# Optimization experiments

Measured on AMD Instinct MI355X. Metric: run time of the kernel, lower is better.

## Reference

```python
import jax, jax.numpy as jnp
import numpy as np

N_NODES, N_EDGES, N_ROOTS = 32768, 131072, 1024
VOCAB, EMB_D, FEAT = 50000, 256, 128
SEQ, HEADS, OUT_CH = 16, 16, 125
KERNELS = (5, 6, 7, 8)


def _add_self_loops(edge_index, n):
    loop = jnp.arange(n, dtype=edge_index.dtype)
    src = jnp.concatenate([edge_index[0], loop])
    dst = jnp.concatenate([edge_index[1], loop])
    return src, dst


def _gat_conv(x, W, a_src, a_dst, b, src, dst, n):
    # PyG GATConv (heads=1): h=xW, e_ij = LeakyReLU(a_s.h_j + a_d.h_i), softmax over incoming edges of i
    h = x @ W                                   # [N, F]
    al_s = h @ a_src                            # [N]
    al_d = h @ a_dst                            # [N]
    e = jax.nn.leaky_relu(al_s[src] + al_d[dst], 0.2)   # [E+N]
    m = jax.ops.segment_max(e, dst, num_segments=n)
    ex = jnp.exp(e - m[dst])
    den = jax.ops.segment_sum(ex, dst, num_segments=n)
    coef = ex / den[dst]
    out = jax.ops.segment_sum(coef[:, None] * h[src], dst, num_segments=n)
    return out + b


def _gcn_conv(x, W, b, src, dst, n):
    h = x @ W
    ones = jnp.ones_like(src, dtype=x.dtype)
    deg = jax.ops.segment_sum(ones, dst, num_segments=n)
    dinv = jax.lax.rsqrt(jnp.maximum(deg, 1.0))
    norm = dinv[src] * dinv[dst]                # [E+N]
    out = jax.ops.segment_sum(norm[:, None] * h[src], dst, num_segments=n)
    return out + b


def _transformer_block(x, Wq, bq, Wk, bk, Wv, bv, Wo, bo, g, be):
    # multi-head self-attention + output proj + residual + layernorm (attn_dropout=0)
    n, s, d = x.shape
    dh = d // HEADS
    q = (x @ Wq + bq).reshape(n, s, HEADS, dh)
    k = (x @ Wk + bk).reshape(n, s, HEADS, dh)
    v = (x @ Wv + bv).reshape(n, s, HEADS, dh)
    att = jnp.einsum('nqhd,nkhd->nhqk', q, k) / np.sqrt(dh).astype(np.float32)
    att = jax.nn.softmax(att, axis=-1)
    o = jnp.einsum('nhqk,nkhd->nqhd', att, v).reshape(n, s, d)
    o = o @ Wo + bo
    y = x + o
    mu = jnp.mean(y, axis=-1, keepdims=True)
    var = jnp.var(y, axis=-1, keepdims=True)
    return (y - mu) * jax.lax.rsqrt(var + 1e-5) * g + be


def _conv_branch(t, ws, bs):
    # t: [N, D, S]; Conv1d VALID + ReLU + max-pool over full output length
    feats = []
    for w, b in zip(ws, bs):
        a = jax.lax.conv_general_dilated(t, w, (1,), 'VALID',
                                         dimension_numbers=('NCH', 'OIH', 'NCH'))
        a = jax.nn.relu(a + b[:, None])
        feats.append(jnp.max(a, axis=-1))       # [N, OUT_CH]
    return jnp.concatenate(feats, axis=1)        # [N, 4*OUT_CH]


def _forward(x2, emb, Wq, bq, Wk, bk, Wv, bv, Wo, bo, ln_g, ln_b,
             gat1_W, gat1_as, gat1_ad, gat1_b, gcn1_W, gcn1_b,
             gat2_W, gat2_as, gat2_ad, gat2_b, gcn2_W, gcn2_b,
             conv_w0, conv_b0, conv_w1, conv_b1, conv_w2, conv_b2, conv_w3, conv_b3,
             fc1_W, fc1_b, fc2_W, fc2_b,
             text2, edge_index, root_index, rootpost_index):
    n = x2.shape[0]
    src, dst = _add_self_loops(edge_index, n)

    stance_graph = _gat_conv(x2, gat1_W, gat1_as, gat1_ad, gat1_b, src, dst, n)
    stance_shared = _gcn_conv(x2, gcn1_W, gcn1_b, src, dst, n)

    t = emb[text2]                                            # [N, S, D]
    t = _transformer_block(t, Wq, bq, Wk, bk, Wv, bv, Wo, bo, ln_g, ln_b)
    t_avg = jnp.mean(t, axis=1)                               # [N, D]

    cat = jnp.concatenate([stance_graph, stance_shared, t_avg], axis=1)  # [N, 2F+D]
    stance_graph2 = _gat_conv(cat, gat2_W, gat2_as, gat2_ad, gat2_b, src, dst, n)
    _ = _gcn_conv(stance_shared, gcn2_W, gcn2_b, src, dst, n)  # computed but unused in forward (faithful)

    tc = jnp.transpose(t, (0, 2, 1))                          # [N, D, S]
    text_feat = _conv_branch(tc, (conv_w0, conv_w1, conv_w2, conv_w3),
                             (conv_b0, conv_b1, conv_b2, conv_b3))  # [N, 500]

    final = jnp.concatenate([stance_graph2[root_index],
                             text_feat[root_index],
                             text_feat[rootpost_index]], axis=1)     # [B, F+1000]
    h = jax.nn.relu(final @ fc1_W + fc1_b)
    return h @ fc2_W + fc2_b                                  # [B, 3]


def setup_inputs() -> dict:
    key = jax.random.key(0)
    ks = iter(jax.random.split(key, 48))
    s = 0.05
    inp = {}
    inp['x2'] = jax.random.normal(next(ks), (N_NODES, FEAT), jnp.float32)
    inp['emb'] = jax.random.normal(next(ks), (VOCAB, EMB_D), jnp.float32) * s
    for nm in ['Wq', 'Wk', 'Wv', 'Wo']:
        inp[nm] = jax.random.normal(next(ks), (EMB_D, EMB_D), jnp.float32) * s
    for nm in ['bq', 'bk', 'bv', 'bo']:
        inp[nm] = jnp.zeros((EMB_D,), jnp.float32)
    inp['ln_g'] = jnp.ones((EMB_D,), jnp.float32)
    inp['ln_b'] = jnp.zeros((EMB_D,), jnp.float32)
    inp['gat1_W'] = jax.random.normal(next(ks), (FEAT, FEAT), jnp.float32) * s
    inp['gat1_as'] = jax.random.normal(next(ks), (FEAT,), jnp.float32) * s
    inp['gat1_ad'] = jax.random.normal(next(ks), (FEAT,), jnp.float32) * s
    inp['gat1_b'] = jnp.zeros((FEAT,), jnp.float32)
    inp['gcn1_W'] = jax.random.normal(next(ks), (FEAT, FEAT), jnp.float32) * s
    inp['gcn1_b'] = jnp.zeros((FEAT,), jnp.float32)
    inp['gat2_W'] = jax.random.normal(next(ks), (2 * FEAT + EMB_D, FEAT), jnp.float32) * s
    inp['gat2_as'] = jax.random.normal(next(ks), (FEAT,), jnp.float32) * s
    inp['gat2_ad'] = jax.random.normal(next(ks), (FEAT,), jnp.float32) * s
    inp['gat2_b'] = jnp.zeros((FEAT,), jnp.float32)
    inp['gcn2_W'] = jax.random.normal(next(ks), (FEAT, FEAT), jnp.float32) * s
    inp['gcn2_b'] = jnp.zeros((FEAT,), jnp.float32)
    for i, K in enumerate(KERNELS):
        inp[f'conv_w{i}'] = jax.random.normal(next(ks), (OUT_CH, EMB_D, K), jnp.float32) * s
        inp[f'conv_b{i}'] = jnp.zeros((OUT_CH,), jnp.float32)
    inp['fc1_W'] = jax.random.normal(next(ks), (FEAT + 8 * OUT_CH, 300), jnp.float32) * s
    inp['fc1_b'] = jnp.zeros((300,), jnp.float32)
    inp['fc2_W'] = jax.random.normal(next(ks), (300, 3), jnp.float32) * s
    inp['fc2_b'] = jnp.zeros((3,), jnp.float32)
    inp['text2'] = jax.random.randint(next(ks), (N_NODES, SEQ), 0, VOCAB, jnp.int32)
    inp['edge_index'] = jax.random.randint(next(ks), (2, N_EDGES), 0, N_NODES, jnp.int32)
    inp['root_index'] = jax.random.randint(next(ks), (N_ROOTS,), 0, N_NODES, jnp.int32)
    inp['rootpost_index'] = jax.random.randint(next(ks), (N_ROOTS,), 0, N_NODES, jnp.int32)
    return inp


def reference(x2, emb, Wq, bq, Wk, bk, Wv, bv, Wo, bo, ln_g, ln_b,
              gat1_W, gat1_as, gat1_ad, gat1_b, gcn1_W, gcn1_b,
              gat2_W, gat2_as, gat2_ad, gat2_b, gcn2_W, gcn2_b,
              conv_w0, conv_b0, conv_w1, conv_b1, conv_w2, conv_b2, conv_w3, conv_b3,
              fc1_W, fc1_b, fc2_W, fc2_b,
              text2, edge_index, root_index, rootpost_index):
    return _forward(x2, emb, Wq, bq, Wk, bk, Wv, bv, Wo, bo, ln_g, ln_b,
                    gat1_W, gat1_as, gat1_ad, gat1_b, gcn1_W, gcn1_b,
                    gat2_W, gat2_as, gat2_ad, gat2_b, gcn2_W, gcn2_b,
                    conv_w0, conv_b0, conv_w1, conv_b1, conv_w2, conv_b2, conv_w3, conv_b3,
                    fc1_W, fc1_b, fc2_W, fc2_b,
                    text2, edge_index, root_index, rootpost_index)
```

## Files before the change

kernel.cpp:

```cpp
#include <hip/hip_runtime.h>
#include <hip/hip_bf16.h>
#include <cstdint>
#include <cstddef>

#define N_NODES 32768
#define N_EDGES 131072
#define ET_EDGES (N_EDGES + N_NODES)
#define N_ROOTS 1024
#define EMB_D 256
#define FEAT 128
#define SEQ 16
#define OUT_CH 125

static inline int cdiv(long long a, long long b) { return (int)((a + b - 1) / b); }

typedef short short8 __attribute__((ext_vector_type(8)));
typedef short short4v __attribute__((ext_vector_type(4)));
typedef float f32x4 __attribute__((ext_vector_type(4)));

__device__ __forceinline__ float warpReduceSum(float v) {
#pragma unroll
    for (int m = 32; m; m >>= 1) v += __shfl_xor(v, m, 64);
    return v;
}
__device__ __forceinline__ int encf(float f) {
    int i = __float_as_int(f);
    return i >= 0 ? i : (i ^ 0x7fffffff);
}
__device__ __forceinline__ float decf(int i) {
    return __int_as_float(i >= 0 ? i : (i ^ 0x7fffffff));
}
__device__ __forceinline__ short f2bs(float x) {
    unsigned u = __float_as_uint(x);
    u += 0x7fffu + ((u >> 16) & 1u);
    return (short)(u >> 16);
}
__device__ __forceinline__ short2 f2bs2(float a, float b) {
    union {
        __hip_bfloat162 h;
        short2 s;
    } u;
    u.h = __float22bfloat162_rn(make_float2(a, b));
    return u.s;
}
__device__ __forceinline__ float bs2f(short s) {
    return __uint_as_float(((unsigned)(unsigned short)s) << 16);
}

__global__ void fill_i32(int* p, int v, int n) {
    int i = blockIdx.x * 256 + threadIdx.x;
    if (i < n) p[i] = v;
}

__global__ void init_cat(float* __restrict__ cat, const float* __restrict__ b1, const float* __restrict__ b2) {
    int i = blockIdx.x * 256 + threadIdx.x;
    int n = i >> 8, c = i & 255;
    float b = (c < 128) ? b1[c] : b2[c - 128];
    cat[(size_t)n * 512 + c] = b;
}

__global__ void repack_wall(const float* __restrict__ cw0, const float* __restrict__ cw1,
                            const float* __restrict__ cw2, const float* __restrict__ cw3,
                            __hip_bfloat16* __restrict__ wall) {
    int i = blockIdx.x * 256 + threadIdx.x;
    if (i >= 512 * 2048) return;
    int r = i >> 11, c = i & 2047;
    int k = c >> 8, ic = c & 255;
    float v = 0.f;
    if (r < 500) {
        int Kidx = r / 125, oc = r - Kidx * 125;
        int K = 5 + Kidx;
        if (k < K) {
            const float* cw = Kidx == 0 ? cw0 : Kidx == 1 ? cw1 : Kidx == 2 ? cw2 : cw3;
            v = cw[((size_t)oc * 256 + ic) * K + k];
        }
    }
    wall[i] = __float2bfloat16(v);
}

__global__ void repack_xf(const float* __restrict__ Wq, const float* __restrict__ Wk, const float* __restrict__ Wv,
                          const float* __restrict__ Wo, const float* __restrict__ bq, const float* __restrict__ bk,
                          const float* __restrict__ bv, short* __restrict__ wqkvT, short* __restrict__ woT,
                          float* __restrict__ bqkv) {
    int i = blockIdx.x * 256 + threadIdx.x;
    if (i < 768 * 256) {
        int n = i >> 8, k = i & 255;
        const float* W = n < 256 ? Wq : n < 512 ? Wk : Wv;
        wqkvT[i] = f2bs(W[k * 256 + (n & 255)]);
    }
    if (i < 256 * 256) {
        int n = i >> 8, k = i & 255;
        woT[i] = f2bs(Wo[k * 256 + n]);
    }
    if (i < 768) bqkv[i] = i < 256 ? bq[i] : i < 512 ? bk[i - 256] : bv[i - 512];
}

__global__ void repack_wT(const float* __restrict__ W, short* __restrict__ out, int K, int N) {
    int i = blockIdx.x * 256 + threadIdx.x;
    if (i >= K * N) return;
    int n = i / K, k = i - n * K;
    out[i] = f2bs(W[(size_t)k * N + n]);
}

__global__ __launch_bounds__(256) void mfma_gemm_n128(const float* __restrict__ A, const short* __restrict__ Wt,
                                                      float* __restrict__ C, int K) {
    __shared__ short As[128 * 40];
    __shared__ short Bs[128 * 40];
    const int m0 = blockIdx.x * 128;
    const int tid = threadIdx.x;
    const int lane = tid & 63;
    const int wave = tid >> 6;
    const int wm = (wave >> 1) * 64, wn = (wave & 1) * 64;
    const int quad = lane >> 4, l16 = lane & 15;

    const int r0 = tid >> 2, kc = (tid & 3) * 8;
    const int r1 = r0 + 64;

    f32x4 acc[4][4];
#pragma unroll
    for (int i = 0; i < 4; i++)
#pragma unroll
        for (int j = 0; j < 4; j++) acc[i][j] = (f32x4){0.f, 0.f, 0.f, 0.f};

    for (int k0 = 0; k0 < K; k0 += 32) {
#pragma unroll
        for (int rr = 0; rr < 2; rr++) {
            const int r = rr ? r1 : r0;
            const float* pa = A + (size_t)(m0 + r) * K + k0 + kc;
            float4 a0 = ((const float4*)pa)[0], a1 = ((const float4*)pa)[1];
            short2 c0 = f2bs2(a0.x, a0.y), c1 = f2bs2(a0.z, a0.w), c2 = f2bs2(a1.x, a1.y), c3 = f2bs2(a1.z, a1.w);
            *(short8*)(As + r * 40 + kc) = (short8){c0.x, c0.y, c1.x, c1.y, c2.x, c2.y, c3.x, c3.y};
        }
        *(short8*)(Bs + r0 * 40 + kc) = *(const short8*)(Wt + (size_t)r0 * K + k0 + kc);
        *(short8*)(Bs + r1 * 40 + kc) = *(const short8*)(Wt + (size_t)r1 * K + k0 + kc);
        __syncthreads();
        short8 af[4], bfr[4];
#pragma unroll
        for (int i = 0; i < 4; i++) af[i] = *(const short8*)(As + (wm + i * 16 + l16) * 40 + quad * 8);
#pragma unroll
        for (int j = 0; j < 4; j++) bfr[j] = *(const short8*)(Bs + (wn + j * 16 + l16) * 40 + quad * 8);
#pragma unroll
        for (int i = 0; i < 4; i++)
#pragma unroll
            for (int j = 0; j < 4; j++)
                acc[i][j] = __builtin_amdgcn_mfma_f32_16x16x32_bf16(af[i], bfr[j], acc[i][j], 0, 0, 0);
        __syncthreads();
    }
#pragma unroll
    for (int i = 0; i < 4; i++) {
#pragma unroll
        for (int j = 0; j < 4; j++) {
            const int col = wn + j * 16 + l16;
            const size_t base = (size_t)(m0 + wm + i * 16 + quad * 4) * 128 + col;
#pragma unroll
            for (int r = 0; r < 4; r++) C[base + (size_t)r * 128] = acc[i][j][r];
        }
    }
}

__global__ __launch_bounds__(256) void gemm64(const float* __restrict__ A, const float* __restrict__ B,
                                              const float* __restrict__ bias, float* __restrict__ C,
                                              int M, int N, int K, int lda, int ldc, int doRelu) {
    __shared__ float As[16][65];
    __shared__ float Bs[16][65];
    const int bm = blockIdx.y * 64, bn = blockIdx.x * 64;
    const int tid = threadIdx.x;
    const int tx = tid & 15, ty = tid >> 4;
    float acc[4][4] = {};
    for (int k0 = 0; k0 < K; k0 += 16) {
#pragma unroll
        for (int j = 0; j < 4; j++) {
            int i = tid + j * 256;
            int kk = i & 15, m = i >> 4;
            int gr = bm + m, gc = k0 + kk;
            As[kk][m] = (gr < M && gc < K) ? A[(size_t)gr * lda + gc] : 0.f;
        }
#pragma unroll
        for (int j = 0; j < 4; j++) {
            int i = tid + j * 256;
            int n = i & 63, kk = i >> 6;
            int gr = k0 + kk, gc = bn + n;
            Bs[kk][n] = (gr < K && gc < N) ? B[(size_t)gr * N + gc] : 0.f;
        }
        __syncthreads();
#pragma unroll
        for (int kk = 0; kk < 16; kk++) {
            float a[4], b[4];
#pragma unroll
            for (int i2 = 0; i2 < 4; i2++) a[i2] = As[kk][ty * 4 + i2];
#pragma unroll
            for (int j2 = 0; j2 < 4; j2++) b[j2] = Bs[kk][tx * 4 + j2];
#pragma unroll
            for (int i2 = 0; i2 < 4; i2++)
#pragma unroll
                for (int j2 = 0; j2 < 4; j2++) acc[i2][j2] = fmaf(a[i2], b[j2], acc[i2][j2]);
        }
        __syncthreads();
    }
#pragma unroll
    for (int i2 = 0; i2 < 4; i2++) {
        int r = bm + ty * 4 + i2;
        if (r >= M) continue;
#pragma unroll
        for (int j2 = 0; j2 < 4; j2++) {
            int c = bn + tx * 4 + j2;
            if (c >= N) continue;
            float v = acc[i2][j2];
            if (bias) v += bias[c];
            if (doRelu) v = fmaxf(v, 0.f);
            C[(size_t)r * ldc + c] = v;
        }
    }
}

__global__ __launch_bounds__(256) void alpha_kernel(const float* __restrict__ h, const float* __restrict__ asrc,
                                                    const float* __restrict__ adst, float* __restrict__ als,
                                                    float* __restrict__ ald) {
    int gw = (blockIdx.x * 256 + threadIdx.x) >> 6;
    int lane = threadIdx.x & 63;
    if (gw >= N_NODES) return;
    const float* row = h + (size_t)gw * FEAT;
    float v0 = row[lane], v1 = row[lane + 64];
    float ps = v0 * asrc[lane] + v1 * asrc[lane + 64];
    float pd = v0 * adst[lane] + v1 * adst[lane + 64];
    ps = warpReduceSum(ps);
    pd = warpReduceSum(pd);
    if (lane == 0) {
        als[gw] = ps;
        ald[gw] = pd;
    }
}

__device__ __forceinline__ void edge_decode(int i, const int* __restrict__ ei, int& s, int& d) {
    if (i < N_EDGES) {
        s = ei[i];
        d = ei[N_EDGES + i];
    } else {
        s = d = i - N_EDGES;
    }
}

__global__ void edge_p1(const int* __restrict__ ei, const float* __restrict__ als, const float* __restrict__ ald,
                        float* __restrict__ elog, int* __restrict__ menc, float* dega) {
    int i = blockIdx.x * 256 + threadIdx.x;
    if (i >= ET_EDGES) return;
    int s, d;
    edge_decode(i, ei, s, d);
    float e = als[s] + ald[d];
    e = (e >= 0.f) ? e : 0.2f * e;
    elog[i] = e;
    atomicMax(&menc[d], encf(e));
    if (dega) unsafeAtomicAdd(&dega[d], 1.f);
}

__global__ void edge_p2(const int* __restrict__ ei, float* __restrict__ elog, const int* __restrict__ menc,
                        float* __restrict__ den) {
    int i = blockIdx.x * 256 + threadIdx.x;
    if (i >= ET_EDGES) return;
    int s, d;
    edge_decode(i, ei, s, d);
    float ex = __expf(elog[i] - decf(menc[d]));
    elog[i] = ex;
    unsafeAtomicAdd(&den[d], ex);
}

__global__ void edge_p2b(const int* __restrict__ ei, float* __restrict__ elog, const float* __restrict__ den) {
    int i = blockIdx.x * 256 + threadIdx.x;
    if (i >= ET_EDGES) return;
    int s, d;
    edge_decode(i, ei, s, d);
    elog[i] = elog[i] / den[d];
}

__global__ void dinv_kernel(float* deg) {
    int i = blockIdx.x * 256 + threadIdx.x;
    if (i < N_NODES) deg[i] = rsqrtf(fmaxf(deg[i], 1.f));
}

__global__ void edge_scatter(const int* __restrict__ ei, const float* __restrict__ coef, const float* __restrict__ h,
                             float* __restrict__ out, int ldo) {
    int i = blockIdx.x * 256 + threadIdx.x;
    if (i >= ET_EDGES * FEAT) return;
    int e = i >> 7, f = i & 127;
    int s, d;
    edge_decode(e, ei, s, d);
    unsafeAtomicAdd(&out[(size_t)d * ldo + f], coef[e] * h[(size_t)s * FEAT + f]);
}

__global__ void gcn_scatter(const int* __restrict__ ei, const float* __restrict__ dinv, const float* __restrict__ h,
                            float* __restrict__ out, int ldo) {
    int i = blockIdx.x * 256 + threadIdx.x;
    if (i >= ET_EDGES * FEAT) return;
    int e = i >> 7, f = i & 127;
    int s, d;
    edge_decode(e, ei, s, d);
    float coef = dinv[s] * dinv[d];
    unsafeAtomicAdd(&out[(size_t)d * ldo + f], coef * h[(size_t)s * FEAT + f]);
}

__global__ void root_gather(const float* __restrict__ g2, const int* __restrict__ rooti, const float* __restrict__ gb,
                            float* __restrict__ fin) {
    int i = blockIdx.x * 256 + threadIdx.x;
    if (i >= N_ROOTS * FEAT) return;
    int r = i >> 7, c = i & 127;
    fin[(size_t)r * 1128 + c] = g2[(size_t)rooti[r] * FEAT + c] + gb[c];
}

__global__ void fc2_kernel(const float* __restrict__ fch, const float* __restrict__ W, const float* __restrict__ b,
                           float* __restrict__ out) {
    int i = blockIdx.x * 256 + threadIdx.x;
    if (i >= N_ROOTS * 3) return;
    int r = i / 3, c = i - r * 3;
    float acc = b[c];
    for (int k = 0; k < 300; k++) acc = fmaf(fch[(size_t)r * 300 + k], W[k * 3 + c], acc);
    out[i] = acc;
}

__device__ __forceinline__ int lsw(int row, int col) {
    return row * 256 + (col ^ ((row & 7) << 3));
}

__device__ __forceinline__ int vt_addr(int d, int key) {
    return d * 32 + (((key & 24) ^ (((d ^ (d >> 2)) & 3) << 3)) | (key & 7));
}

template <int MODE>
__global__ __launch_bounds__(256, 4) void xformer_kernel(
    const float* __restrict__ emb, const int* __restrict__ text2, const short* __restrict__ wqkvT,
    const float* __restrict__ bqkv, const short* __restrict__ woT, const float* __restrict__ bo,
    const float* __restrict__ lng, const float* __restrict__ lnb, const int* __restrict__ rooti,
    const int* __restrict__ rpi, float* __restrict__ cat, unsigned short* __restrict__ tbuf) {
    __shared__ short qa[32 * 256];
    __shared__ short kreg[32 * 256];
    __shared__ short vbuf[32 * 256];

    const int tid = threadIdx.x;
    const int wave = tid >> 6, lane = tid & 63;
    const int quad = lane >> 4, l16 = lane & 15;

    int gnode[2];
#pragma unroll
    for (int m = 0; m < 2; m++) {
        int slot = blockIdx.x * 2 + m;
        gnode[m] = (MODE == 0) ? slot : ((slot < N_ROOTS) ? rooti[slot] : rpi[slot - N_ROOTS]);
    }

    {
        const int row = tid >> 3, seg = tid & 7;
        const int m = row >> 4, r = row & 15;
        const int tok = text2[gnode[m] * SEQ + r];
        const float* ep = emb + (size_t)tok * 256 + seg * 32;
#pragma unroll
        for (int j = 0; j < 4; j++) {
            float4 ea = ((const float4*)(ep + j * 8))[0];
            float4 eb = ((const float4*)(ep + j * 8))[1];
            short2 w0 = f2bs2(ea.x, ea.y), w1 = f2bs2(ea.z, ea.w);
            short2 w2 = f2bs2(eb.x, eb.y), w3 = f2bs2(eb.z, eb.w);
            *(short8*)(kreg + lsw(row, seg * 32 + j * 8)) =
                (short8){w0.x, w0.y, w1.x, w1.y, w2.x, w2.y, w3.x, w3.y};
        }
    }
    __syncthreads();

    auto run_gemm = [&](const short* __restrict__ W, int wrow0, const short* __restrict__ Albase,
                        f32x4(&acc)[4][2]) {
#pragma unroll
        for (int i = 0; i < 4; i++) {
            acc[i][0] = (f32x4){0.f, 0.f, 0.f, 0.f};
            acc[i][1] = (f32x4){0.f, 0.f, 0.f, 0.f};
        }
        const short* wb = W + (size_t)(wrow0 + l16) * 256 + quad * 8;
        short8 Bcur[4], Bnxt[4];
#pragma unroll
        for (int i = 0; i < 4; i++) Bcur[i] = *(const short8*)(wb + (size_t)i * 16 * 256);
#pragma unroll
        for (int k0 = 0; k0 < 8; k0++) {
            if (k0 < 7) {
#pragma unroll
                for (int i = 0; i < 4; i++)
                    Bnxt[i] = *(const short8*)(wb + (size_t)i * 16 * 256 + (k0 + 1) * 32);
            }
            short8 A0 = *(const short8*)(Albase + lsw(l16, k0 * 32 + quad * 8));
            short8 A1 = *(const short8*)(Albase + lsw(16 + l16, k0 * 32 + quad * 8));
#pragma unroll
            for (int i = 0; i < 4; i++) {
                acc[i][0] = __builtin_amdgcn_mfma_f32_16x16x32_bf16(A0, Bcur[i], acc[i][0], 0, 0, 0);
                acc[i][1] = __builtin_amdgcn_mfma_f32_16x16x32_bf16(A1, Bcur[i], acc[i][1], 0, 0, 0);
            }
#pragma unroll
            for (int i = 0; i < 4; i++) Bcur[i] = Bnxt[i];
        }
    };

    {
        f32x4 acc[4][2];
        run_gemm(wqkvT, (0 * 16 + wave * 4) * 16, kreg, acc);
#pragma unroll
        for (int i = 0; i < 4; i++) {
            const int col = (wave * 4 + i) * 16 + l16;
            const float b = bqkv[col];
#pragma unroll
            for (int m = 0; m < 2; m++) {
                const int rbase = m * 16 + quad * 4;
                short2 p01 = f2bs2((acc[i][m][0] + b) * 0.25f, (acc[i][m][1] + b) * 0.25f);
                short2 p23 = f2bs2((acc[i][m][2] + b) * 0.25f, (acc[i][m][3] + b) * 0.25f);
                qa[lsw(rbase + 0, col)] = p01.x;
                qa[lsw(rbase + 1, col)] = p01.y;
                qa[lsw(rbase + 2, col)] = p23.x;
                qa[lsw(rbase + 3, col)] = p23.y;
            }
        }
        f32x4 kacc[4][2];
        run_gemm(wqkvT, (1 * 16 + wave * 4) * 16, kreg, kacc);
#pragma unroll
        for (int i = 0; i < 4; i++) {
            const int colg = (1 * 16 + wave * 4 + i) * 16 + l16;
            const float b = bqkv[colg];
            const int cl = colg - 256;
#pragma unroll
            for (int m = 0; m < 2; m++) {
                const int rbase = m * 16 + quad * 4;
                short2 p01 = f2bs2(kacc[i][m][0] + b, kacc[i][m][1] + b);
                short2 p23 = f2bs2(kacc[i][m][2] + b, kacc[i][m][3] + b);
                vbuf[lsw(rbase + 0, cl)] = p01.x;
                vbuf[lsw(rbase + 1, cl)] = p01.y;
                vbuf[lsw(rbase + 2, cl)] = p23.x;
                vbuf[lsw(rbase + 3, cl)] = p23.y;
            }
        }
        f32x4 vacc[4][2];
        run_gemm(wqkvT, (2 * 16 + wave * 4) * 16, kreg, vacc);
        __syncthreads();
#pragma unroll
        for (int i = 0; i < 4; i++) {
            const int d = (wave * 4 + i) * 16 + l16;
            const float b = bqkv[(2 * 16 + wave * 4 + i) * 16 + l16];
#pragma unroll
            for (int m = 0; m < 2; m++) {
                const int rbase = m * 16 + quad * 4;
                short2 p01 = f2bs2(vacc[i][m][0] + b, vacc[i][m][1] + b);
                short2 p23 = f2bs2(vacc[i][m][2] + b, vacc[i][m][3] + b);
                *(short4v*)(kreg + vt_addr(d, rbase)) = (short4v){p01.x, p01.y, p23.x, p23.y};
            }
        }
    }

#pragma unroll
    for (int p = 0; p < 2; p++) {
#pragma unroll
        for (int i = 0; i < 4; i++) {
            const int h = wave * 4 + i;
            const int arow = p * 16 + l16;
            const int q8 = (quad & 1) * 8;
            short8 Af = *(const short8*)(vbuf + lsw(arow, h * 16 + q8));
            short8 Bf = *(const short8*)(qa + lsw(arow, h * 16 + q8));
            if (quad >= 2) {
                Af = (short8){0, 0, 0, 0, 0, 0, 0, 0};
                Bf = (short8){0, 0, 0, 0, 0, 0, 0, 0};
            }
            f32x4 S = __builtin_amdgcn_mfma_f32_16x16x32_bf16(Af, Bf, (f32x4){0.f, 0.f, 0.f, 0.f}, 0, 0, 0);
            float mx = fmaxf(fmaxf(S[0], S[1]), fmaxf(S[2], S[3]));
            mx = fmaxf(mx, __shfl_xor(mx, 16));
            mx = fmaxf(mx, __shfl_xor(mx, 32));
            float e0 = __expf(S[0] - mx), e1 = __expf(S[1] - mx);
            float e2 = __expf(S[2] - mx), e3 = __expf(S[3] - mx);
            float sm = (e0 + e1) + (e2 + e3);
            sm += __shfl_xor(sm, 16);
            sm += __shfl_xor(sm, 32);
            const float inv = 1.f / sm;
            short2 p01 = f2bs2(e0 * inv, e1 * inv), p23 = f2bs2(e2 * inv, e3 * inv);
            *(short4v*)(qa + lsw(arow, h * 16 + quad * 4)) = (short4v){p01.x, p01.y, p23.x, p23.y};
        }
    }

#pragma unroll
    for (int p = 0; p < 2; p++) {
#pragma unroll
        for (int i = 0; i < 4; i++) {
            const int h = wave * 4 + i;
            const int arow = p * 16 + l16;
            const int q8 = (quad & 1) * 8;
            short8 BP = *(const short8*)(qa + lsw(arow, h * 16 + q8));
            short8 Av = *(const short8*)(kreg + vt_addr(h * 16 + l16, p * 16 + q8));
            if (quad >= 2) {
                BP = (short8){0, 0, 0, 0, 0, 0, 0, 0};
                Av = (short8){0, 0, 0, 0, 0, 0, 0, 0};
            }
            f32x4 O = __builtin_amdgcn_mfma_f32_16x16x32_bf16(Av, BP, (f32x4){0.f, 0.f, 0.f, 0.f}, 0, 0, 0);
            short2 o01 = f2bs2(O[0], O[1]), o23 = f2bs2(O[2], O[3]);
            *(short4v*)(qa + lsw(arow, h * 16 + quad * 4)) = (short4v){o01.x, o01.y, o23.x, o23.y};
        }
    }
    __syncthreads();

    {
        f32x4 oacc[4][2];
        run_gemm(woT, (wave * 4) * 16, qa, oacc);
#pragma unroll
        for (int i = 0; i < 4; i++) {
            const int col = (wave * 4 + i) * 16 + l16;
            const float bocol = bo[col];
#pragma unroll
            for (int m = 0; m < 2; m++) {
                const int rbase = m * 16 + quad * 4;
                short2 a01 = f2bs2(oacc[i][m][0] + bocol, oacc[i][m][1] + bocol);
                short2 a23 = f2bs2(oacc[i][m][2] + bocol, oacc[i][m][3] + bocol);
                kreg[lsw(rbase + 0, col)] = a01.x;
                kreg[lsw(rbase + 1, col)] = a01.y;
                kreg[lsw(rbase + 2, col)] = a23.x;
                kreg[lsw(rbase + 3, col)] = a23.y;
            }
        }
    }
    __syncthreads();

    float* qs = (float*)qa;
    {
        const int row = tid >> 3, seg = tid & 7;
        const int m = row >> 4, r = row & 15;
        const int tokr = text2[gnode[m] * SEQ + r];
        const float* ep = emb + (size_t)tokr * 256 + seg * 32;
        float sum = 0.f, sq = 0.f;
#pragma unroll
        for (int j = 0; j < 4; j++) {
            const int base = lsw(row, seg * 32 + j * 8);
            short8 y8 = *(const short8*)(kreg + base);
            float4 ea = ((const float4*)(ep + j * 8))[0];
            float4 eb = ((const float4*)(ep + j * 8))[1];
            float evv[8] = {ea.x, ea.y, ea.z, ea.w, eb.x, eb.y, eb.z, eb.w};
            float yv[8];
#pragma unroll
            for (int e = 0; e < 8; e++) {
                yv[e] = bs2f(y8[e]) + evv[e];
                sum += yv[e];
                sq = fmaf(yv[e], yv[e], sq);
            }
            short2 w0 = f2bs2(yv[0], yv[1]), w1 = f2bs2(yv[2], yv[3]);
            short2 w2 = f2bs2(yv[4], yv[5]), w3 = f2bs2(yv[6], yv[7]);
            *(short4v*)(kreg + base) = (short4v){w0.x, w0.y, w1.x, w1.y};
            *(short4v*)(kreg + base + 4) = (short4v){w2.x, w2.y, w3.x, w3.y};
        }
        qs[tid] = sum;
        qs[256 + tid] = sq;
    }
    __syncthreads();
    if (tid < 32) {
        float s = 0.f, q2 = 0.f;
#pragma unroll
        for (int j = 0; j < 8; j++) {
            s += qs[tid * 8 + j];
            q2 += qs[256 + tid * 8 + j];
        }
        float mu = s * (1.f / 256.f);
        float var = q2 * (1.f / 256.f) - mu * mu;
        qs[512 + tid * 2] = mu;
        qs[512 + tid * 2 + 1] = rsqrtf(var + 1e-5f);
    }
    __syncthreads();
    {
        const int c = tid;
        const float g = lng[c], bb = lnb[c];
        float csum[2] = {0.f, 0.f};
#pragma unroll
        for (int m = 0; m < 2; m++) {
#pragma unroll
            for (int r = 0; r < 16; r++) {
                const int row = m * 16 + r;
                const float yv = bs2f(kreg[lsw(row, c)]);
                const float mu = qs[512 + row * 2], rstd = qs[512 + row * 2 + 1];
                const float o = (yv - mu) * rstd * g + bb;
                if (MODE == 0) {
                    csum[m] += o;
                } else {
                    tbuf[((size_t)(blockIdx.x * 2 + m) * 24 + r) * 256 + c] = (unsigned short)f2bs(o);
                }
            }
        }
        if (MODE == 0) {
            cat[(size_t)gnode[0] * 512 + 256 + c] = csum[0] * (1.f / 16.f);
            cat[(size_t)gnode[1] * 512 + 256 + c] = csum[1] * (1.f / 16.f);
        } else {
            for (int z = tid; z < 2 * 8 * 256; z += 256) {
                const int m = z >> 11, rem = z & 2047;
                tbuf[((size_t)(blockIdx.x * 2 + m) * 24 + 16 + (rem >> 8)) * 256 + (rem & 255)] = 0;
            }
        }
    }
}

__global__ __launch_bounds__(256) void conv_gemm(const short* __restrict__ tb, const short* __restrict__ wall,
                                                 float* __restrict__ C) {
    __shared__ short As[128 * 40];
    __shared__ short Bs[128 * 40];
    const int bid = blockIdx.x;
    const int m0 = (bid >> 2) * 128;
    const int n0 = (bid & 3) * 128;
    const int tid = threadIdx.x;
    const int lane = tid & 63;
    const int wave = tid >> 6;
    const int wm = (wave >> 1) * 64, wn = (wave & 1) * 64;
    const int quad = lane >> 4, l16 = lane & 15;

    const int r0 = tid >> 2, kc = (tid & 3) * 8;
    const int r1 = r0 + 64;
    const int am0 = m0 + r0, am1 = m0 + r1;
    const int s0 = am0 / 12, p0_ = am0 - s0 * 12;
    const int s1 = am1 / 12, p1_ = am1 - s1 * 12;
    const size_t ga0 = (size_t)(s0 * 24 + p0_) * 256 + kc;
    const size_t ga1 = (size_t)(s1 * 24 + p1_) * 256 + kc;
    const size_t gb0 = (size_t)(n0 + r0) * 2048 + kc;
    const size_t gb1 = (size_t)(n0 + r1) * 2048 + kc;
    short* sa0 = As + r0 * 40 + kc;
    short* sa1 = As + r1 * 40 + kc;
    short* sb0 = Bs + r0 * 40 + kc;
    short* sb1 = Bs + r1 * 40 + kc;

    f32x4 acc[4][4];
#pragma unroll
    for (int i = 0; i < 4; i++)
#pragma unroll
        for (int j = 0; j < 4; j++) acc[i][j] = (f32x4){0.f, 0.f, 0.f, 0.f};

    for (int k0 = 0; k0 < 2048; k0 += 32) {
        short8 a0 = *(const short8*)(tb + ga0 + k0);
        short8 a1 = *(const short8*)(tb + ga1 + k0);
        short8 b0 = *(const short8*)(wall + gb0 + k0);
        short8 b1 = *(const short8*)(wall + gb1 + k0);
        *(short8*)sa0 = a0;
        *(short8*)sa1 = a1;
        *(short8*)sb0 = b0;
        *(short8*)sb1 = b1;
        __syncthreads();
        short8 af[4], bfr[4];
#pragma unroll
        for (int i = 0; i < 4; i++) af[i] = *(const short8*)(As + (wm + i * 16 + l16) * 40 + quad * 8);
#pragma unroll
        for (int j = 0; j < 4; j++) bfr[j] = *(const short8*)(Bs + (wn + j * 16 + l16) * 40 + quad * 8);
#pragma unroll
        for (int i = 0; i < 4; i++)
#pragma unroll
            for (int j = 0; j < 4; j++)
                acc[i][j] = __builtin_amdgcn_mfma_f32_16x16x32_bf16(af[i], bfr[j], acc[i][j], 0, 0, 0);
        __syncthreads();
    }
#pragma unroll
    for (int i = 0; i < 4; i++) {
#pragma unroll
        for (int j = 0; j < 4; j++) {
            const int col = n0 + wn + j * 16 + l16;
            const size_t base = (size_t)(m0 + wm + i * 16 + quad * 4) * 512 + col;
#pragma unroll
            for (int r = 0; r < 4; r++) C[base + (size_t)r * 512] = acc[i][j][r];
        }
    }
}

__global__ void conv_maxpool(const float* __restrict__ C, const float* __restrict__ cb0, const float* __restrict__ cb1,
                             const float* __restrict__ cb2, const float* __restrict__ cb3, float* __restrict__ fin) {
    int i = blockIdx.x * 256 + threadIdx.x;
    if (i >= 2048 * 500) return;
    int slot = i / 500, q = i - slot * 500;
    int Kidx = q / 125, oc = q - Kidx * 125;
    int L = 12 - Kidx;
    const float* base = C + (size_t)(slot * 12) * 512 + q;
    float m = base[0];
    for (int p = 1; p < L; p++) m = fmaxf(m, base[(size_t)p * 512]);
    float b = (Kidx == 0 ? cb0 : Kidx == 1 ? cb1 : Kidx == 2 ? cb2 : cb3)[oc];
    float v = fmaxf(m + b, 0.f);
    int idx = slot < N_ROOTS ? slot : slot - N_ROOTS;
    int colbase = slot < N_ROOTS ? 128 : 628;
    fin[(size_t)idx * 1128 + colbase + q] = v;
}

extern "C" void kernel_launch(void* const* d_in, const int* in_sizes, int n_in, void* d_out, int out_size, void* d_ws,
                              size_t ws_size, hipStream_t stream) {
    const float* x2 = (const float*)d_in[0];
    const float* emb = (const float*)d_in[1];
    const float* Wq = (const float*)d_in[2];
    const float* Wk = (const float*)d_in[3];
    const float* Wv = (const float*)d_in[4];
    const float* Wo = (const float*)d_in[5];
    const float* bq = (const float*)d_in[6];
    const float* bk = (const float*)d_in[7];
    const float* bv = (const float*)d_in[8];
    const float* bo = (const float*)d_in[9];
    const float* lng = (const float*)d_in[10];
    const float* lnb = (const float*)d_in[11];
    const float* gat1_W = (const float*)d_in[12];
    const float* gat1_as = (const float*)d_in[13];
    const float* gat1_ad = (const float*)d_in[14];
    const float* gat1_b = (const float*)d_in[15];
    const float* gcn1_W = (const float*)d_in[16];
    const float* gcn1_b = (const float*)d_in[17];
    const float* gat2_W = (const float*)d_in[18];
    const float* gat2_as = (const float*)d_in[19];
    const float* gat2_ad = (const float*)d_in[20];
    const float* gat2_b = (const float*)d_in[21];
    const float* cw0 = (const float*)d_in[24];
    const float* cb0 = (const float*)d_in[25];
    const float* cw1 = (const float*)d_in[26];
    const float* cb1 = (const float*)d_in[27];
    const float* cw2 = (const float*)d_in[28];
    const float* cb2 = (const float*)d_in[29];
    const float* cw3 = (const float*)d_in[30];
    const float* cb3 = (const float*)d_in[31];
    const float* fc1_W = (const float*)d_in[32];
    const float* fc1_b = (const float*)d_in[33];
    const float* fc2_W = (const float*)d_in[34];
    const float* fc2_b = (const float*)d_in[35];
    const int* text2 = (const int*)d_in[36];
    const int* ei = (const int*)d_in[37];
    const int* rooti = (const int*)d_in[38];
    const int* rpi = (const int*)d_in[39];

    float* ws = (float*)d_ws;
    size_t off = 0;
    auto alloc = [&](size_t n) {
        float* p = ws + off;
        off += n;
        return p;
    };
    float* g2o = alloc((size_t)N_NODES * FEAT);
    float* den1 = alloc(N_NODES);
    float* den2 = alloc(N_NODES);
    float* deg = alloc(N_NODES);
    size_t zero_floats = off;
    float* cat = alloc((size_t)N_NODES * 512);
    float* h1 = alloc((size_t)N_NODES * FEAT);
    float* h2 = alloc((size_t)N_NODES * FEAT);
    float* hg2 = alloc((size_t)N_NODES * FEAT);
    float* als1 = alloc(N_NODES);
    float* ald1 = alloc(N_NODES);
    float* als2 = alloc(N_NODES);
    float* ald2 = alloc(N_NODES);
    int* m1 = (int*)alloc(N_NODES);
    int* m2 = (int*)alloc(N_NODES);
    float* el1 = alloc(ET_EDGES);
    float* el2 = alloc(ET_EDGES);
    float* fin = alloc((size_t)N_ROOTS * 1128);
    float* fch = alloc((size_t)N_ROOTS * 300);
    float* wallf = alloc(512 * 2048 / 2);
    float* wqkvTf = alloc(768 * 256 / 2);
    float* woTf = alloc(256 * 256 / 2);
    float* bqkv = alloc(768);
    float* wg1Tf = alloc(128 * 128 / 2);
    float* wc1Tf = alloc(128 * 128 / 2);
    float* wg2Tf = alloc(128 * 512 / 2);
    (void)ws_size;
    (void)in_sizes;
    (void)n_in;
    (void)out_size;

    unsigned short* tbuf = (unsigned short*)h1;
    __hip_bfloat16* wall = (__hip_bfloat16*)wallf;
    short* wqkvT = (short*)wqkvTf;
    short* woT = (short*)woTf;
    short* wg1T = (short*)wg1Tf;
    short* wc1T = (short*)wc1Tf;
    short* wg2T = (short*)wg2Tf;
    float* Cbuf = cat;

    hipMemsetAsync(g2o, 0, zero_floats * sizeof(float), stream);
    init_cat<<<cdiv((long long)N_NODES * 256, 256), 256, 0, stream>>>(cat, gat1_b, gcn1_b);
    fill_i32<<<cdiv(2 * N_NODES, 256), 256, 0, stream>>>(m1, (int)0x80000000, 2 * N_NODES);
    repack_wall<<<cdiv(512 * 2048, 256), 256, 0, stream>>>(cw0, cw1, cw2, cw3, wall);
    repack_xf<<<cdiv(768 * 256, 256), 256, 0, stream>>>(Wq, Wk, Wv, Wo, bq, bk, bv, wqkvT, woT, bqkv);
    repack_wT<<<cdiv(128 * 128, 256), 256, 0, stream>>>(gat1_W, wg1T, 128, 128);
    repack_wT<<<cdiv(128 * 128, 256), 256, 0, stream>>>(gcn1_W, wc1T, 128, 128);
    repack_wT<<<cdiv(512 * 128, 256), 256, 0, stream>>>(gat2_W, wg2T, 512, 128);

    mfma_gemm_n128<<<N_NODES / 128, 256, 0, stream>>>(x2, wg1T, h1, 128);
    mfma_gemm_n128<<<N_NODES / 128, 256, 0, stream>>>(x2, wc1T, h2, 128);
    alpha_kernel<<<cdiv((long long)N_NODES * 64, 256), 256, 0, stream>>>(h1, gat1_as, gat1_ad, als1, ald1);
    edge_p1<<<cdiv(ET_EDGES, 256), 256, 0, stream>>>(ei, als1, ald1, el1, m1, deg);
    edge_p2<<<cdiv(ET_EDGES, 256), 256, 0, stream>>>(ei, el1, m1, den1);
    edge_p2b<<<cdiv(ET_EDGES, 256), 256, 0, stream>>>(ei, el1, den1);
    dinv_kernel<<<cdiv(N_NODES, 256), 256, 0, stream>>>(deg);
    const int sc_blocks = cdiv((long long)ET_EDGES * FEAT, 256);
    edge_scatter<<<sc_blocks, 256, 0, stream>>>(ei, el1, h1, cat + 0, 512);
    gcn_scatter<<<sc_blocks, 256, 0, stream>>>(ei, deg, h2, cat + 128, 512);
    xformer_kernel<0><<<N_NODES / 2, 256, 0, stream>>>(emb, text2, wqkvT, bqkv, woT, bo, lng, lnb, rooti, rpi, cat,
                                                       nullptr);
    xformer_kernel<1><<<2 * N_ROOTS / 2, 256, 0, stream>>>(emb, text2, wqkvT, bqkv, woT, bo, lng, lnb, rooti, rpi,
                                                           nullptr, tbuf);
    mfma_gemm_n128<<<N_NODES / 128, 256, 0, stream>>>(cat, wg2T, hg2, 512);
    alpha_kernel<<<cdiv((long long)N_NODES * 64, 256), 256, 0, stream>>>(hg2, gat2_as, gat2_ad, als2, ald2);
    edge_p1<<<cdiv(ET_EDGES, 256), 256, 0, stream>>>(ei, als2, ald2, el2, m2, nullptr);
    edge_p2<<<cdiv(ET_EDGES, 256), 256, 0, stream>>>(ei, el2, m2, den2);
    edge_p2b<<<cdiv(ET_EDGES, 256), 256, 0, stream>>>(ei, el2, den2);
    edge_scatter<<<sc_blocks, 256, 0, stream>>>(ei, el2, hg2, g2o, FEAT);
    conv_gemm<<<192 * 4, 256, 0, stream>>>((const short*)tbuf, (const short*)wall, Cbuf);
    root_gather<<<cdiv(N_ROOTS * FEAT, 256), 256, 0, stream>>>(g2o, rooti, gat2_b, fin);
    conv_maxpool<<<cdiv(2048 * 500, 256), 256, 0, stream>>>(Cbuf, cb0, cb1, cb2, cb3, fin);
    gemm64<<<dim3(cdiv(300, 64), cdiv(N_ROOTS, 64)), 256, 0, stream>>>(fin, fc1_W, fc1_b, fch, N_ROOTS, 300, 1128,
                                                                       1128, 300, 1);
    fc2_kernel<<<cdiv(N_ROOTS * 3, 256), 256, 0, stream>>>(fch, fc2_W, fc2_b, (float*)d_out);
}
```

Measured before the change: 2.375 ms.

## Split transformer GEMMs into half-width passes and reorder Q/K/V staging

Each projection GEMM now computes two 16-column tiles per pass instead of four, looping twice, which halves the accumulator and prefetch register footprint. K is written to a per-wave private region of vbuf, so scores can be computed before V is projected. V is then projected and transposed into vbuf after the softmax, which removes a block barrier, and the launch bound drops from 4 to 3 blocks per SM. The aim is less register pressure and less synchronisation, at the cost of reloading the A fragments twice per GEMM, less ILP, and a lower occupancy hint.

```diff
diff --git a/kernel.cpp b/kernel.cpp
--- a/kernel.cpp
+++ b/kernel.cpp
@@ -325,7 +325,7 @@
 }
 
 template <int MODE>
-__global__ __launch_bounds__(256, 4) void xformer_kernel(
+__global__ __launch_bounds__(256, 3) void xformer_kernel(
     const float* __restrict__ emb, const int* __restrict__ text2, const short* __restrict__ wqkvT,
     const float* __restrict__ bqkv, const short* __restrict__ woT, const float* __restrict__ bo,
     const float* __restrict__ lng, const float* __restrict__ lnb, const int* __restrict__ rooti,
@@ -362,85 +362,74 @@
     }
     __syncthreads();
 
-    auto run_gemm = [&](const short* __restrict__ W, int wrow0, const short* __restrict__ Albase,
-                        f32x4(&acc)[4][2]) {
-#pragma unroll
-        for (int i = 0; i < 4; i++) {
+    auto run_gemm_h = [&](const short* __restrict__ W, int wrow0, const short* __restrict__ Albase,
+                          f32x4(&acc)[2][2]) {
+#pragma unroll
+        for (int i = 0; i < 2; i++) {
             acc[i][0] = (f32x4){0.f, 0.f, 0.f, 0.f};
             acc[i][1] = (f32x4){0.f, 0.f, 0.f, 0.f};
         }
         const short* wb = W + (size_t)(wrow0 + l16) * 256 + quad * 8;
-        short8 Bcur[4], Bnxt[4];
-#pragma unroll
-        for (int i = 0; i < 4; i++) Bcur[i] = *(const short8*)(wb + (size_t)i * 16 * 256);
+        short8 B0 = *(const short8*)(wb);
+        short8 B1 = *(const short8*)(wb + 16 * 256);
 #pragma unroll
         for (int k0 = 0; k0 < 8; k0++) {
+            short8 B0n, B1n;
             if (k0 < 7) {
-#pragma unroll
-                for (int i = 0; i < 4; i++)
-                    Bnxt[i] = *(const short8*)(wb + (size_t)i * 16 * 256 + (k0 + 1) * 32);
+                B0n = *(const short8*)(wb + (k0 + 1) * 32);
+                B1n = *(const short8*)(wb + 16 * 256 + (k0 + 1) * 32);
             }
             short8 A0 = *(const short8*)(Albase + lsw(l16, k0 * 32 + quad * 8));
             short8 A1 = *(const short8*)(Albase + lsw(16 + l16, k0 * 32 + quad * 8));
-#pragma unroll
-            for (int i = 0; i < 4; i++) {
-                acc[i][0] = __builtin_amdgcn_mfma_f32_16x16x32_bf16(A0, Bcur[i], acc[i][0], 0, 0, 0);
-                acc[i][1] = __builtin_amdgcn_mfma_f32_16x16x32_bf16(A1, Bcur[i], acc[i][1], 0, 0, 0);
-            }
-#pragma unroll
-            for (int i = 0; i < 4; i++) Bcur[i] = Bnxt[i];
+            acc[0][0] = __builtin_amdgcn_mfma_f32_16x16x32_bf16(A0, B0, acc[0][0], 0, 0, 0);
+            acc[0][1] = __builtin_amdgcn_mfma_f32_16x16x32_bf16(A1, B0, acc[0][1], 0, 0, 0);
+            acc[1][0] = __builtin_amdgcn_mfma_f32_16x16x32_bf16(A0, B1, acc[1][0], 0, 0, 0);
+            acc[1][1] = __builtin_amdgcn_mfma_f32_16x16x32_bf16(A1, B1, acc[1][1], 0, 0, 0);
+            B0 = B0n;
+            B1 = B1n;
         }
     };
 
-    {
-        f32x4 acc[4][2];
-        run_gemm(wqkvT, (0 * 16 + wave * 4) * 16, kreg, acc);
-#pragma unroll
-        for (int i = 0; i < 4; i++) {
-            const int col = (wave * 4 + i) * 16 + l16;
+    auto kpriv = [&](int row, int c) { return wave * 2048 + row * 64 + (c ^ ((row & 7) << 3)); };
+
+    f32x4 acc[2][2];
+
+#pragma unroll 1
+    for (int hh = 0; hh < 2; hh++) {
+        run_gemm_h(wqkvT, (wave * 4 + hh * 2) * 16, kreg, acc);
+#pragma unroll
+        for (int ii = 0; ii < 2; ii++) {
+            const int col = (wave * 4 + hh * 2 + ii) * 16 + l16;
             const float b = bqkv[col];
 #pragma unroll
             for (int m = 0; m < 2; m++) {
                 const int rbase = m * 16 + quad * 4;
-                short2 p01 = f2bs2((acc[i][m][0] + b) * 0.25f, (acc[i][m][1] + b) * 0.25f);
-                short2 p23 = f2bs2((acc[i][m][2] + b) * 0.25f, (acc[i][m][3] + b) * 0.25f);
+                short2 p01 = f2bs2((acc[ii][m][0] + b) * 0.25f, (acc[ii][m][1] + b) * 0.25f);
+                short2 p23 = f2bs2((acc[ii][m][2] + b) * 0.25f, (acc[ii][m][3] + b) * 0.25f);
                 qa[lsw(rbase + 0, col)] = p01.x;
                 qa[lsw(rbase + 1, col)] = p01.y;
                 qa[lsw(rbase + 2, col)] = p23.x;
                 qa[lsw(rbase + 3, col)] = p23.y;
             }
         }
-        f32x4 kacc[4][2];
-        run_gemm(wqkvT, (1 * 16 + wave * 4) * 16, kreg, kacc);
-#pragma unroll
-        for (int i = 0; i < 4; i++) {
-            const int colg = (1 * 16 + wave * 4 + i) * 16 + l16;
-            const float b = bqkv[colg];
-            const int cl = colg - 256;
+    }
+#pragma unroll 1
+    for (int hh = 0; hh < 2; hh++) {
+        run_gemm_h(wqkvT, (16 + wave * 4 + hh * 2) * 16, kreg, acc);
+#pragma unroll
+        for (int ii = 0; ii < 2; ii++) {
+            const int i = hh * 2 + ii;
+            const int c = i * 16 + l16;
+            const float b = bqkv[(16 + wave * 4 + i) * 16 + l16];
 #pragma unroll
             for (int m = 0; m < 2; m++) {
                 const int rbase = m * 16 + quad * 4;
-                short2 p01 = f2bs2(kacc[i][m][0] + b, kacc[i][m][1] + b);
-                short2 p23 = f2bs2(kacc[i][m][2] + b, kacc[i][m][3] + b);
-                vbuf[lsw(rbase + 0, cl)] = p01.x;
-                vbuf[lsw(rbase + 1, cl)] = p01.y;
-                vbuf[lsw(rbase + 2, cl)] = p23.x;
-                vbuf[lsw(rbase + 3, cl)] = p23.y;
-            }
-        }
-        f32x4 vacc[4][2];
-        run_gemm(wqkvT, (2 * 16 + wave * 4) * 16, kreg, vacc);
-        __syncthreads();
-#pragma unroll
-        for (int i = 0; i < 4; i++) {
-            const int d = (wave * 4 + i) * 16 + l16;
-            const float b = bqkv[(2 * 16 + wave * 4 + i) * 16 + l16];
-#pragma unroll
-            for (int m = 0; m < 2; m++) {
-                const int rbase = m * 16 + quad * 4;
-                short2 p01 = f2bs2(vacc[i][m][0] + b, vacc[i][m][1] + b);
-                short2 p23 = f2bs2(vacc[i][m][2] + b, vacc[i][m][3] + b);
-                *(short4v*)(kreg + vt_addr(d, rbase)) = (short4v){p01.x, p01.y, p23.x, p23.y};
+                short2 p01 = f2bs2(acc[ii][m][0] + b, acc[ii][m][1] + b);
+                short2 p23 = f2bs2(acc[ii][m][2] + b, acc[ii][m][3] + b);
+                vbuf[kpriv(rbase + 0, c)] = p01.x;
+                vbuf[kpriv(rbase + 1, c)] = p01.y;
+                vbuf[kpriv(rbase + 2, c)] = p23.x;
+                vbuf[kpriv(rbase + 3, c)] = p23.y;
             }
         }
     }
@@ -452,7 +441,7 @@
             const int h = wave * 4 + i;
             const int arow = p * 16 + l16;
             const int q8 = (quad & 1) * 8;
-            short8 Af = *(const short8*)(vbuf + lsw(arow, h * 16 + q8));
+            short8 Af = *(const short8*)(vbuf + kpriv(arow, i * 16 + q8));
             short8 Bf = *(const short8*)(qa + lsw(arow, h * 16 + q8));
             if (quad >= 2) {
                 Af = (short8){0, 0, 0, 0, 0, 0, 0, 0};
@@ -473,6 +462,24 @@
         }
     }
 
+#pragma unroll 1
+    for (int hh = 0; hh < 2; hh++) {
+        run_gemm_h(wqkvT, (32 + wave * 4 + hh * 2) * 16, kreg, acc);
+#pragma unroll
+        for (int ii = 0; ii < 2; ii++) {
+            const int i = hh * 2 + ii;
+            const int d = (wave * 4 + i) * 16 + l16;
+            const float b = bqkv[(32 + wave * 4 + i) * 16 + l16];
+#pragma unroll
+            for (int m = 0; m < 2; m++) {
+                const int rbase = m * 16 + quad * 4;
+                short2 p01 = f2bs2(acc[ii][m][0] + b, acc[ii][m][1] + b);
+                short2 p23 = f2bs2(acc[ii][m][2] + b, acc[ii][m][3] + b);
+                *(short4v*)(vbuf + vt_addr(d, rbase)) = (short4v){p01.x, p01.y, p23.x, p23.y};
+            }
+        }
+    }
+
 #pragma unroll
     for (int p = 0; p < 2; p++) {
 #pragma unroll
@@ -481,7 +488,7 @@
             const int arow = p * 16 + l16;
             const int q8 = (quad & 1) * 8;
             short8 BP = *(const short8*)(qa + lsw(arow, h * 16 + q8));
-            short8 Av = *(const short8*)(kreg + vt_addr(h * 16 + l16, p * 16 + q8));
+            short8 Av = *(const short8*)(vbuf + vt_addr(h * 16 + l16, p * 16 + q8));
             if (quad >= 2) {
                 BP = (short8){0, 0, 0, 0, 0, 0, 0, 0};
                 Av = (short8){0, 0, 0, 0, 0, 0, 0, 0};
@@ -493,18 +500,18 @@
     }
     __syncthreads();
 
-    {
-        f32x4 oacc[4][2];
-        run_gemm(woT, (wave * 4) * 16, qa, oacc);
-#pragma unroll
-        for (int i = 0; i < 4; i++) {
-            const int col = (wave * 4 + i) * 16 + l16;
+#pragma unroll 1
+    for (int hh = 0; hh < 2; hh++) {
+        run_gemm_h(woT, (wave * 4 + hh * 2) * 16, qa, acc);
+#pragma unroll
+        for (int ii = 0; ii < 2; ii++) {
+            const int col = (wave * 4 + hh * 2 + ii) * 16 + l16;
             const float bocol = bo[col];
 #pragma unroll
             for (int m = 0; m < 2; m++) {
                 const int rbase = m * 16 + quad * 4;
-                short2 a01 = f2bs2(oacc[i][m][0] + bocol, oacc[i][m][1] + bocol);
-                short2 a23 = f2bs2(oacc[i][m][2] + bocol, oacc[i][m][3] + bocol);
+                short2 a01 = f2bs2(acc[ii][m][0] + bocol, acc[ii][m][1] + bocol);
+                short2 a23 = f2bs2(acc[ii][m][2] + bocol, acc[ii][m][3] + bocol);
                 kreg[lsw(rbase + 0, col)] = a01.x;
                 kreg[lsw(rbase + 1, col)] = a01.y;
                 kreg[lsw(rbase + 2, col)] = a23.x;
```

After: 2.020 ms. -14.9%, faster.
